# Kernel optimization log

Hardware: AMD Instinct MI355X
Metric: run time of the kernel (lower is better)

## Reference

```python
import jax, jax.numpy as jnp
import numpy as np

B, IN_C, OUT_C, K, Z_DIM = 32, 128, 128, 3, 512
H, W, STRIDE = 56, 56, 1


def setup_inputs() -> dict:
    key = jax.random.key(0)
    k1, k2, k3 = jax.random.split(key, 3)
    x = jax.random.normal(k1, (B, IN_C, H, W), dtype=jnp.float32)
    z = jax.random.normal(k2, (B, Z_DIM), dtype=jnp.float32)
    # nn.Linear(z_dim, out_c*in_c*k*k): weight [out_f, in_f], bias [out_f]
    out_f = OUT_C * IN_C * K * K
    W_head = jax.random.normal(k3, (out_f, Z_DIM), dtype=jnp.float32) * (1.0 / np.sqrt(Z_DIM))
    b_head = jnp.zeros((out_f,), dtype=jnp.float32)
    return {"x": x, "z": z, "W_head": W_head, "b_head": b_head}


def reference(x, z, W_head, b_head):
    b = x.shape[0]
    # hypernetwork head: per-sample conv weights
    w = z @ W_head.T + b_head                       # [B, out_c*in_c*k*k]
    w = w.reshape(b, OUT_C, IN_C, K, K)             # [B, O, I, K, K]

    pad = K // 2

    def conv_one(xi, wi):
        # xi: [I, H, W], wi: [O, I, K, K] -> [O, H', W']
        out = jax.lax.conv_general_dilated(
            xi[None],                                # [1, I, H, W]
            wi,
            window_strides=(STRIDE, STRIDE),
            padding=[(pad, pad), (pad, pad)],
            dimension_numbers=("NCHW", "OIHW", "NCHW"),
        )
        return out[0]

    return jax.vmap(conv_one)(x, w)                 # [B, O, H', W']
```

## Files before the change

kernel.cpp:

```cpp
#include <hip/hip_runtime.h>
#include <hip/hip_bf16.h>
#include <stdint.h>

#define BB 32
#define IC 128
#define OC 128
#define HH 56
#define WW 56
#define ZD 512
#define NRS 9
#define OI (OC*IC)
#define WROWS (OI*NRS)
#define WDIM 58

typedef float  f32x4  __attribute__((ext_vector_type(4)));
typedef short  bf16x8 __attribute__((ext_vector_type(8)));

static __device__ __forceinline__ short f2bf(float f) {
    uint32_t u = __float_as_uint(f);
    uint32_t r = (u + 0x7fffu + ((u >> 16) & 1u)) >> 16;
    return (short)r;
}
static __device__ __forceinline__ short f2bf_hw(float f) {
    __hip_bfloat16 h = __float2bfloat16(f);
    return *reinterpret_cast<short*>(&h);
}
static __device__ __forceinline__ float bf2f(short s) {
    uint32_t u = ((uint32_t)(uint16_t)s) << 16;
    return __uint_as_float(u);
}
static __device__ __forceinline__ void gll16(const void* g, void* l) {
    __builtin_amdgcn_global_load_lds(
        (const __attribute__((address_space(1))) uint32_t*)g,
        (__attribute__((address_space(3))) uint32_t*)l, 16, 0, 0);
}

__global__ __launch_bounds__(256) void head_kernel(
    const float* __restrict__ Wh, const float* __restrict__ z,
    short* __restrict__ wnat)
{
    __shared__ __align__(16) char Zl[32 * 1024];
    __shared__ __align__(16) char Wl[4 * 3 * 8192];
    const int tid  = threadIdx.x;
    const int lane = tid & 63;
    const int wv   = tid >> 6;

    {
        const int b = tid >> 3, ks = (tid & 7) * 64;
        const float* zp = z + (size_t)b * ZD + ks;
        const int bx = (b & 7) << 4;
        #pragma unroll
        for (int j8 = 0; j8 < 8; ++j8) {
            f32x4 v0 = *(const f32x4*)(zp + j8 * 8);
            f32x4 v1 = *(const f32x4*)(zp + j8 * 8 + 4);
            bf16x8 pk;
            pk[0] = f2bf_hw(v0.x); pk[1] = f2bf_hw(v0.y);
            pk[2] = f2bf_hw(v0.z); pk[3] = f2bf_hw(v0.w);
            pk[4] = f2bf_hw(v1.x); pk[5] = f2bf_hw(v1.y);
            pk[6] = f2bf_hw(v1.z); pk[7] = f2bf_hw(v1.w);
            *(bf16x8*)(Zl + b * 1024 + ((ks * 2 + j8 * 16) ^ bx)) = pk;
        }
    }
    __syncthreads();

    const int rl = lane & 15;
    const int kq = lane >> 4;
    const int zxor = (rl & 7) << 4;
    const int q  = lane >> 5;

    uint32_t O[4];
    #pragma unroll
    for (int j = 0; j < 4; ++j)
        O[j] = j * 4096 + q * 2048 +
               (((lane & 31) * 16) ^ (((2 * j + q) & 7) << 4));

    const char* WB = (const char*)Wh +
        (size_t)(blockIdx.x * 576 + wv * 16) * (ZD * 4);
    char* WLb = Wl + wv * 24576;

    #define STAGE(gg, ss, buf)                                                  \
        {                                                                       \
            const char* sb_ = WB + (size_t)(gg) * 131072 + (ss) * 512;          \
            char* db_ = WLb + (buf) * 8192;                                     \
            _Pragma("unroll")                                                   \
            for (int i_ = 0; i_ < 8; ++i_)                                      \
                gll16(sb_ + (i_ >> 2) * 16384 + O[i_ & 3], db_ + i_ * 1024);    \
        }

    STAGE(0, 0, 0);
    STAGE(0, 1, 1);

    int bufc = 0;
    for (int g = 0; g < 9; ++g) {
        f32x4 acc0 = {0.f, 0.f, 0.f, 0.f}, acc1 = {0.f, 0.f, 0.f, 0.f};
        #pragma unroll
        for (int s = 0; s < 4; ++s) {
            if (s == 0) {
                if (g) { asm volatile("s_waitcnt vmcnt(16)" ::: "memory"); }
                else   { asm volatile("s_waitcnt vmcnt(8)"  ::: "memory"); }
            } else if (s == 3) {
                if (g == 8) { asm volatile("s_waitcnt vmcnt(0)" ::: "memory"); }
                else        { asm volatile("s_waitcnt vmcnt(8)" ::: "memory"); }
            } else {
                asm volatile("s_waitcnt vmcnt(8)" ::: "memory");
            }
            __builtin_amdgcn_sched_barrier(0);

            const char* cb = WLb + bufc * 8192;
            #pragma unroll
            for (int j = 0; j < 4; ++j) {
                const int kb = s * 4 + j;
                const int koff = (kb * 64 + kq * 16) ^ zxor;
                bf16x8 a0 = *(const bf16x8*)(Zl + rl * 1024 + koff);
                bf16x8 a1 = *(const bf16x8*)(Zl + (16 + rl) * 1024 + koff);
                f32x4 lo = *(const f32x4*)(cb + rl * 512 + ((j * 128 + kq * 32) ^ zxor));
                f32x4 hi = *(const f32x4*)(cb + rl * 512 + ((j * 128 + kq * 32 + 16) ^ zxor));
                bf16x8 bw;
                bw[0] = f2bf_hw(lo.x); bw[1] = f2bf_hw(lo.y);
                bw[2] = f2bf_hw(lo.z); bw[3] = f2bf_hw(lo.w);
                bw[4] = f2bf_hw(hi.x); bw[5] = f2bf_hw(hi.y);
                bw[6] = f2bf_hw(hi.z); bw[7] = f2bf_hw(hi.w);
                acc0 = __builtin_amdgcn_mfma_f32_16x16x32_bf16(a0, bw, acc0, 0, 0, 0);
                acc1 = __builtin_amdgcn_mfma_f32_16x16x32_bf16(a1, bw, acc1, 0, 0, 0);
            }

            if (s == 3) {
                const int rowg = blockIdx.x * 576 + g * 64 + wv * 16 + rl;
                #pragma unroll
                for (int reg = 0; reg < 4; ++reg) {
                    const int b0 = kq * 4 + reg;
                    wnat[(size_t)b0 * WROWS + rowg]        = f2bf(acc0[reg]);
                    wnat[(size_t)(16 + b0) * WROWS + rowg] = f2bf(acc1[reg]);
                }
            }

            {
                const int su = 4 * g + s + 2;
                if (su < 36) {
                    const int sbuf = (bufc + 2) % 3;
                    const int gg = g + (s >= 2 ? 1 : 0);
                    const int ss = (s + 2) & 3;
                    STAGE(gg, ss, sbuf);
                }
            }
            bufc = (bufc == 2) ? 0 : bufc + 1;
        }
    }
    #undef STAGE
}

__global__ __launch_bounds__(256) void repack_kernel(
    const short* __restrict__ wnat, const float* __restrict__ bh,
    short* __restrict__ wbf)
{
    const int b = blockIdx.y;
    const int oi0 = blockIdx.x * 2048 + threadIdx.x * 8;
    const short* src = wnat + (size_t)b * WROWS + (size_t)oi0 * 9;
    const float* bp  = bh + (size_t)oi0 * 9;

    bf16x8 in[9];
    #pragma unroll
    for (int j = 0; j < 9; ++j) in[j] = *(const bf16x8*)(src + j * 8);
    f32x4 bv[18];
    #pragma unroll
    for (int m = 0; m < 18; ++m) bv[m] = *(const f32x4*)(bp + m * 4);

    #pragma unroll
    for (int rs = 0; rs < 9; ++rs) {
        bf16x8 o;
        #pragma unroll
        for (int jj = 0; jj < 8; ++jj) {
            const int e = jj * 9 + rs;
            float v = bf2f(in[e >> 3][e & 7]) + bv[e >> 2][e & 3];
            o[jj] = f2bf(v);
        }
        *(bf16x8*)(wbf + ((size_t)(b * 9 + rs)) * OI + oi0) = o;
    }
}

__global__ __launch_bounds__(256) void transpose_kernel(
    const float* __restrict__ x, short* __restrict__ xt)
{
    const int h = blockIdx.x;
    const int b = blockIdx.y;
    const int w = threadIdx.x & 63;
    const int yq = threadIdx.x >> 6;
    if (w >= WW) return;
    const float* xp = x + (size_t)b * IC * HH * WW + h * WW + w;
    short* op = xt + (((size_t)(b * HH + h)) * WW + w) * IC;
    #pragma unroll
    for (int q = 0; q < 4; ++q) {
        int ic = yq * 4 + q;
        bf16x8 pk;
        #pragma unroll
        for (int j = 0; j < 8; ++j) {
            float v = xp[(size_t)(ic * 8 + j) * (HH * WW)];
            pk[j] = f2bf(v);
        }
        *(bf16x8*)(op + ic * 8) = pk;
    }
}

__global__ __launch_bounds__(256) void conv_kernel(
    const short* __restrict__ wbf,
    const short* __restrict__ xt,
    float* __restrict__ out)
{
    __shared__ __align__(16) char Xl[3 * WDIM * 256];
    __shared__ __align__(16) char Wl[128 * 256];
    const int tid  = threadIdx.x;
    const int lane = tid & 63;
    const int wv   = tid >> 6;
    const int h = blockIdx.x;
    const int b = blockIdx.y;

    #pragma unroll
    for (int q = 0; q < 11; ++q) {
        int idx = tid + q * 256;
        if (idx < 3 * WDIM * 16) ((f32x4*)Xl)[idx] = (f32x4){0.f, 0.f, 0.f, 0.f};
    }
    __syncthreads();

    for (int r = 0; r < 3; ++r) {
        int hin = h + r - 1;
        if (hin < 0 || hin >= HH) continue;
        const char* src = (const char*)(xt + ((size_t)(b * HH + hin)) * WW * IC);
        char* dstbase = Xl + (r * WDIM + 1) * 256;
        for (int it = wv; it < 14; it += 4) {
            int c = it * 64 + lane;
            int u = r * WDIM + 1 + (c >> 4);
            int soff = (c * 16) ^ ((u & 7) << 4);
            gll16(src + soff, dstbase + it * 1024);
        }
    }

    f32x4 acc[2][4];
    #pragma unroll
    for (int a = 0; a < 2; ++a)
        #pragma unroll
        for (int p = 0; p < 4; ++p) acc[a][p] = (f32x4){0.f, 0.f, 0.f, 0.f};

    const int axor = (lane & 7) << 4;
    int kkoff[4];
    #pragma unroll
    for (int kk = 0; kk < 4; ++kk) kkoff[kk] = kk * 64 + ((lane >> 4) << 4);

    for (int rs = 0; rs < 9; ++rs) {
        __syncthreads();
        const char* wsrc = (const char*)(wbf + ((size_t)b * NRS + rs) * OI);
        for (int it = wv; it < 32; it += 4) {
            int c = it * 64 + lane;
            int soff = (c * 16) ^ (((c >> 4) & 7) << 4);
            gll16(wsrc + soff, Wl + it * 1024);
        }
        __syncthreads();

        const int r = rs / 3, s = rs - 3 * (rs / 3);
        int ubase[4], bswz[4];
        #pragma unroll
        for (int pf = 0; pf < 4; ++pf) {
            int p = pf * 16 + (lane & 15);
            int pc = p > 55 ? 55 : p;
            int uu = r * WDIM + pc + s;
            ubase[pf] = uu * 256;
            bswz[pf] = (uu & 7) << 4;
        }
        #pragma unroll
        for (int kk = 0; kk < 4; ++kk) {
            bf16x8 a0 = *(const bf16x8*)(Wl + (wv * 32 + (lane & 15)) * 256 +
                                         (kkoff[kk] ^ axor));
            bf16x8 a1 = *(const bf16x8*)(Wl + (wv * 32 + 16 + (lane & 15)) * 256 +
                                         (kkoff[kk] ^ axor));
            #pragma unroll
            for (int pf = 0; pf < 4; ++pf) {
                bf16x8 bv = *(const bf16x8*)(Xl + ubase[pf] + (kkoff[kk] ^ bswz[pf]));
                acc[0][pf] = __builtin_amdgcn_mfma_f32_16x16x32_bf16(a0, bv, acc[0][pf], 0, 0, 0);
                acc[1][pf] = __builtin_amdgcn_mfma_f32_16x16x32_bf16(a1, bv, acc[1][pf], 0, 0, 0);
            }
        }
    }

    const int pcol = lane & 15;
    const int rowq = lane >> 4;
    #pragma unroll
    for (int a = 0; a < 2; ++a) {
        int o0 = wv * 32 + a * 16 + rowq * 4;
        #pragma unroll
        for (int pf = 0; pf < 4; ++pf) {
            int p = pf * 16 + pcol;
            if (p < WW) {
                #pragma unroll
                for (int reg = 0; reg < 4; ++reg) {
                    out[(((size_t)b * OC + (o0 + reg)) * HH + h) * WW + p] = acc[a][pf][reg];
                }
            }
        }
    }
}

extern "C" void kernel_launch(void* const* d_in, const int* in_sizes, int n_in,
                              void* d_out, int out_size, void* d_ws, size_t ws_size,
                              hipStream_t stream) {
    const float* x  = (const float*)d_in[0];
    const float* z  = (const float*)d_in[1];
    const float* Wh = (const float*)d_in[2];
    const float* bh = (const float*)d_in[3];
    float* out = (float*)d_out;

    short* wnat = (short*)d_ws;
    short* wbf  = (short*)((char*)d_ws + 9437184);
    short* xt   = (short*)((char*)d_ws + 18874368);

    head_kernel<<<dim3(256), 256, 0, stream>>>(Wh, z, wnat);
    repack_kernel<<<dim3(8, 32), 256, 0, stream>>>(wnat, bh, wbf);
    transpose_kernel<<<dim3(HH, BB), 256, 0, stream>>>(x, xt);
    conv_kernel<<<dim3(HH, BB), 256, 0, stream>>>(wbf, xt, out);
}
```

Baseline: 164.5 us.

## Spread hypernetwork head GEMM over many more blocks with register-staged double buffering

The head GEMM previously used 256 blocks, each looping over 9 row groups with a triple-buffered global_load_lds pipeline and hand-tuned waitcnts. Now each block computes a single 64-row tile, giving 2304 blocks. W_head is staged through registers into a double-buffered swizzled LDS tile with one chunk of prefetch. The aim is more parallelism and occupancy across the GPU for this bandwidth-bound 37 MB weight read. In exchange, the async LDS loads are dropped and the z tile is reconverted to bf16 in every block.

New measurement: 168.9 us. +2.6%, slower.

```diff
diff --git a/kernel.cpp b/kernel.cpp
--- a/kernel.cpp
+++ b/kernel.cpp
@@ -40,7 +40,7 @@
     short* __restrict__ wnat)
 {
     __shared__ __align__(16) char Zl[32 * 1024];
-    __shared__ __align__(16) char Wl[4 * 3 * 8192];
+    __shared__ __align__(16) char Wl[4][2][4096];
     const int tid  = threadIdx.x;
     const int lane = tid & 63;
     const int wv   = tid >> 6;
@@ -66,87 +66,68 @@
     const int rl = lane & 15;
     const int kq = lane >> 4;
     const int zxor = (rl & 7) << 4;
-    const int q  = lane >> 5;
-
-    uint32_t O[4];
-    #pragma unroll
-    for (int j = 0; j < 4; ++j)
-        O[j] = j * 4096 + q * 2048 +
-               (((lane & 31) * 16) ^ (((2 * j + q) & 7) << 4));
-
-    const char* WB = (const char*)Wh +
-        (size_t)(blockIdx.x * 576 + wv * 16) * (ZD * 4);
-    char* WLb = Wl + wv * 24576;
-
-    #define STAGE(gg, ss, buf)                                                  \
-        {                                                                       \
-            const char* sb_ = WB + (size_t)(gg) * 131072 + (ss) * 512;          \
-            char* db_ = WLb + (buf) * 8192;                                     \
-            _Pragma("unroll")                                                   \
-            for (int i_ = 0; i_ < 8; ++i_)                                      \
-                gll16(sb_ + (i_ >> 2) * 16384 + O[i_ & 3], db_ + i_ * 1024);    \
-        }
-
-    STAGE(0, 0, 0);
-    STAGE(0, 1, 1);
-
-    int bufc = 0;
-    for (int g = 0; g < 9; ++g) {
-        f32x4 acc0 = {0.f, 0.f, 0.f, 0.f}, acc1 = {0.f, 0.f, 0.f, 0.f};
-        #pragma unroll
-        for (int s = 0; s < 4; ++s) {
-            if (s == 0) {
-                if (g) { asm volatile("s_waitcnt vmcnt(16)" ::: "memory"); }
-                else   { asm volatile("s_waitcnt vmcnt(8)"  ::: "memory"); }
-            } else if (s == 3) {
-                if (g == 8) { asm volatile("s_waitcnt vmcnt(0)" ::: "memory"); }
-                else        { asm volatile("s_waitcnt vmcnt(8)" ::: "memory"); }
-            } else {
-                asm volatile("s_waitcnt vmcnt(8)" ::: "memory");
-            }
-            __builtin_amdgcn_sched_barrier(0);
-
-            const char* cb = WLb + bufc * 8192;
-            #pragma unroll
-            for (int j = 0; j < 4; ++j) {
-                const int kb = s * 4 + j;
-                const int koff = (kb * 64 + kq * 16) ^ zxor;
-                bf16x8 a0 = *(const bf16x8*)(Zl + rl * 1024 + koff);
-                bf16x8 a1 = *(const bf16x8*)(Zl + (16 + rl) * 1024 + koff);
-                f32x4 lo = *(const f32x4*)(cb + rl * 512 + ((j * 128 + kq * 32) ^ zxor));
-                f32x4 hi = *(const f32x4*)(cb + rl * 512 + ((j * 128 + kq * 32 + 16) ^ zxor));
-                bf16x8 bw;
-                bw[0] = f2bf_hw(lo.x); bw[1] = f2bf_hw(lo.y);
-                bw[2] = f2bf_hw(lo.z); bw[3] = f2bf_hw(lo.w);
-                bw[4] = f2bf_hw(hi.x); bw[5] = f2bf_hw(hi.y);
-                bw[6] = f2bf_hw(hi.z); bw[7] = f2bf_hw(hi.w);
-                acc0 = __builtin_amdgcn_mfma_f32_16x16x32_bf16(a0, bw, acc0, 0, 0, 0);
-                acc1 = __builtin_amdgcn_mfma_f32_16x16x32_bf16(a1, bw, acc1, 0, 0, 0);
-            }
-
-            if (s == 3) {
-                const int rowg = blockIdx.x * 576 + g * 64 + wv * 16 + rl;
-                #pragma unroll
-                for (int reg = 0; reg < 4; ++reg) {
-                    const int b0 = kq * 4 + reg;
-                    wnat[(size_t)b0 * WROWS + rowg]        = f2bf(acc0[reg]);
-                    wnat[(size_t)(16 + b0) * WROWS + rowg] = f2bf(acc1[reg]);
-                }
-            }
-
-            {
-                const int su = 4 * g + s + 2;
-                if (su < 36) {
-                    const int sbuf = (bufc + 2) % 3;
-                    const int gg = g + (s >= 2 ? 1 : 0);
-                    const int ss = (s + 2) & 3;
-                    STAGE(gg, ss, sbuf);
-                }
-            }
-            bufc = (bufc == 2) ? 0 : bufc + 1;
-        }
-    }
-    #undef STAGE
+    const int row0 = blockIdx.x * 64 + wv * 16;
+
+    const float* lsrc = Wh + (size_t)(row0 + kq) * ZD + (lane & 15) * 4;
+    char* WT = (char*)Wl[wv][0];
+
+    #define LOADC(c, R)                                                         \
+        _Pragma("unroll")                                                       \
+        for (int j = 0; j < 4; ++j)                                             \
+            R[j] = *(const f32x4*)(lsrc + (size_t)(j * 4) * ZD + (c) * 64);
+
+    #define WRC(buf, R)                                                         \
+        _Pragma("unroll")                                                       \
+        for (int j = 0; j < 4; ++j) {                                           \
+            const int row_ = j * 4 + kq;                                        \
+            *(f32x4*)(WT + (buf) * 4096 + row_ * 256 +                          \
+                      (((lane & 15) * 16) ^ ((row_ & 7) << 4))) = R[j];         \
+        }
+
+    f32x4 RA[4], RB[4];
+    LOADC(0, RA);
+    LOADC(1, RB);
+    WRC(0, RA);
+
+    f32x4 acc0 = {0.f, 0.f, 0.f, 0.f}, acc1 = {0.f, 0.f, 0.f, 0.f};
+
+    #pragma unroll
+    for (int c = 0; c < 8; ++c) {
+        if (c + 2 < 8) {
+            if ((c & 1) == 0) { LOADC(c + 2, RA); }
+            else              { LOADC(c + 2, RB); }
+        }
+        #pragma unroll
+        for (int ks = 0; ks < 2; ++ks) {
+            const int koff = (c * 128 + ks * 64 + kq * 16) ^ zxor;
+            bf16x8 a0 = *(const bf16x8*)(Zl + rl * 1024 + koff);
+            bf16x8 a1 = *(const bf16x8*)(Zl + (16 + rl) * 1024 + koff);
+            const char* wb = WT + (c & 1) * 4096 + rl * 256;
+            f32x4 lo = *(const f32x4*)(wb + ((ks * 128 + kq * 32) ^ zxor));
+            f32x4 hi = *(const f32x4*)(wb + ((ks * 128 + kq * 32 + 16) ^ zxor));
+            bf16x8 bw;
+            bw[0] = f2bf_hw(lo.x); bw[1] = f2bf_hw(lo.y);
+            bw[2] = f2bf_hw(lo.z); bw[3] = f2bf_hw(lo.w);
+            bw[4] = f2bf_hw(hi.x); bw[5] = f2bf_hw(hi.y);
+            bw[6] = f2bf_hw(hi.z); bw[7] = f2bf_hw(hi.w);
+            acc0 = __builtin_amdgcn_mfma_f32_16x16x32_bf16(a0, bw, acc0, 0, 0, 0);
+            acc1 = __builtin_amdgcn_mfma_f32_16x16x32_bf16(a1, bw, acc1, 0, 0, 0);
+        }
+        if (c + 1 < 8) {
+            if ((c & 1) == 0) { WRC(1, RB); }
+            else              { WRC(0, RA); }
+        }
+    }
+    #undef LOADC
+    #undef WRC
+
+    const int rowg = row0 + rl;
+    #pragma unroll
+    for (int reg = 0; reg < 4; ++reg) {
+        const int b0 = kq * 4 + reg;
+        wnat[(size_t)b0 * WROWS + rowg]        = f2bf(acc0[reg]);
+        wnat[(size_t)(16 + b0) * WROWS + rowg] = f2bf(acc1[reg]);
+    }
 }
 
 __global__ __launch_bounds__(256) void repack_kernel(
@@ -311,7 +292,7 @@
     short* wbf  = (short*)((char*)d_ws + 9437184);
     short* xt   = (short*)((char*)d_ws + 18874368);
 
-    head_kernel<<<dim3(256), 256, 0, stream>>>(Wh, z, wnat);
+    head_kernel<<<dim3(WROWS / 64), 256, 0, stream>>>(Wh, z, wnat);
     repack_kernel<<<dim3(8, 32), 256, 0, stream>>>(wnat, bh, wbf);
     transpose_kernel<<<dim3(HH, BB), 256, 0, stream>>>(x, xt);
     conv_kernel<<<dim3(HH, BB), 256, 0, stream>>>(wbf, xt, out);
```
